# Kernel tuning notes

Measured on AMD Instinct MI355X. Metric: run time of the kernel, lower is better.

The kernel has to match this reference:

```python
import jax, jax.numpy as jnp
import numpy as np

NUM_USERS = 100000
NUM_ITEMS = 50000
N_TOTAL = NUM_USERS + NUM_ITEMS
NNZ = 4000000
LATENT_DIM = 64
N_LAYERS = 3
BATCH = 16384


def setup_inputs() -> dict:
    key = jax.random.key(0)
    k1, k2, k3, k4, k5, k6, k7 = jax.random.split(key, 7)
    return {
        "user_emb": jax.random.normal(k1, (NUM_USERS, LATENT_DIM), dtype=jnp.float32) * 0.1,
        "item_emb": jax.random.normal(k2, (NUM_ITEMS, LATENT_DIM), dtype=jnp.float32) * 0.1,
        "vals": jax.random.uniform(k3, (NNZ,), dtype=jnp.float32),
        "rows": jax.random.randint(k4, (NNZ,), 0, N_TOTAL, dtype=jnp.int32),
        "cols": jax.random.randint(k5, (NNZ,), 0, N_TOTAL, dtype=jnp.int32),
        "users": jax.random.randint(k6, (BATCH,), 0, NUM_USERS, dtype=jnp.int64),
        "items": jax.random.randint(k7, (BATCH,), 0, NUM_ITEMS, dtype=jnp.int64),
    }


def _spmm(vals, rows, cols, x):
    # sparse.mm(A, x) with A given as COO edge list: out[r] += vals * x[c]
    return jax.ops.segment_sum(vals[:, None] * x[cols], rows, num_segments=N_TOTAL)


def reference(user_emb, item_emb, vals, rows, cols, users, items):
    # LightGCN.computer(): multi-hop propagation + mean over layer outputs
    all_emb = jnp.concatenate([user_emb, item_emb], axis=0)  # [N+M, d]
    acc = all_emb
    emb = all_emb
    for _ in range(N_LAYERS):
        emb = _spmm(vals, rows, cols, emb)
        acc = acc + emb
    light_out = acc / jnp.asarray(N_LAYERS + 1, dtype=acc.dtype)
    all_users = light_out[:NUM_USERS]
    all_items = light_out[NUM_USERS:]
    # forward(users, items): gather and elementwise dot product
    u = all_users[users]  # [B, d]
    i = all_items[items]  # [B, d]
    gamma = jnp.sum(u * i, axis=1)  # [B]
    return gamma
```

## Files before the change

### kernel.cpp

```cpp
#include <hip/hip_runtime.h>

#define NUM_USERS 100000
#define NUM_ITEMS 50000
#define N_TOTAL   150000
#define LATENT    64
#define BATCH     16384
#define BROWS     512
#define NB        293
#define CAP       16384
#define P1_T      512
#define P1_C      4096

typedef unsigned int u32;
typedef unsigned short u16;

__device__ __forceinline__ u16 f32_to_bf16(float f) {
    u32 u = __float_as_uint(f);
    u32 r = (u + 0x7FFFu + ((u >> 16) & 1u)) >> 16;
    return (u16)r;
}
__device__ __forceinline__ float bf16_lo(u32 w) { return __uint_as_float(w << 16); }
__device__ __forceinline__ float bf16_hi(u32 w) { return __uint_as_float(w & 0xFFFF0000u); }

__device__ __forceinline__ void fma4(float acc[4], uint2 xv, float v) {
    acc[0] = fmaf(v, bf16_lo(xv.x), acc[0]);
    acc[1] = fmaf(v, bf16_hi(xv.x), acc[1]);
    acc[2] = fmaf(v, bf16_lo(xv.y), acc[2]);
    acc[3] = fmaf(v, bf16_hi(xv.y), acc[3]);
}

__device__ __forceinline__ int wave_incl_scan(int v, int lane) {
    #pragma unroll
    for (int d = 1; d < 64; d <<= 1) {
        int t = __shfl_up(v, d, 64);
        if (lane >= d) v += t;
    }
    return v;
}

__device__ __forceinline__ int block_excl_scan_512(int v, int t, int* wsum) {
    int lane = t & 63, w = t >> 6;
    int incl = wave_incl_scan(v, lane);
    if (lane == 63) wsum[w] = incl;
    __syncthreads();
    if (t == 0) {
        int acc = 0;
        #pragma unroll
        for (int k = 0; k < 8; ++k) { int c = wsum[k]; wsum[k] = acc; acc += c; }
    }
    __syncthreads();
    return wsum[w] + incl - v;
}

__global__ void __launch_bounds__(P1_T)
partition1_kernel(const int* __restrict__ rows, const int* __restrict__ cols,
                  const float* __restrict__ vals,
                  int* __restrict__ ccur, uint2* __restrict__ packed0,
                  u16* __restrict__ klab, int nnz) {
    __shared__ u32 skey[P1_C];
    __shared__ u32 sval[P1_C];
    __shared__ u16 sbucket[P1_C];
    __shared__ int cnt[NB];
    __shared__ int lstart[NB];
    __shared__ int lcur[NB];
    __shared__ int gbase[NB];
    __shared__ int wsum[8];

    int t = threadIdx.x;
    int base = blockIdx.x * P1_C;
    int chunkN = nnz - base; if (chunkN > P1_C) chunkN = P1_C;

    for (int i = t; i < NB; i += P1_T) cnt[i] = 0;
    __syncthreads();

    int er[8]; u32 ek[8]; u32 ev[8];
    #pragma unroll
    for (int k = 0; k < 8; ++k) {
        int e = base + k * P1_T + t;
        bool ok = (k * P1_T + t) < chunkN;
        int r = ok ? rows[e] : 0;
        er[k] = ok ? (r >> 9) : -1;
        if (ok) {
            ek[k] = (u32)cols[e] | ((u32)(r & (BROWS - 1)) << 18);
            ev[k] = __float_as_uint(vals[e]);
            atomicAdd(&cnt[er[k]], 1);
        }
    }
    __syncthreads();

    int v = (t < NB) ? cnt[t] : 0;
    int excl = block_excl_scan_512(v, t, wsum);
    if (t < NB) {
        lstart[t] = excl;
        lcur[t] = excl;
        gbase[t] = v ? atomicAdd(&ccur[t], v) : 0;
    }
    __syncthreads();

    #pragma unroll
    for (int k = 0; k < 8; ++k) {
        if (er[k] >= 0) {
            int pos = atomicAdd(&lcur[er[k]], 1);
            skey[pos] = ek[k];
            sval[pos] = ev[k];
            sbucket[pos] = (u16)er[k];
        }
    }
    __syncthreads();

    for (int idx = t; idx < chunkN; idx += P1_T) {
        int b2 = sbucket[idx];
        size_t gp = (size_t)b2 * CAP + gbase[b2] + (idx - lstart[b2]);
        u32 key = skey[idx];
        packed0[gp] = make_uint2(key, sval[idx]);
        klab[gp] = (u16)(key >> 18);
    }
}

__global__ void bucket_scan_kernel(const int* __restrict__ ccur, int* __restrict__ cptr,
                                   int* __restrict__ rowptr, int nnz) {
    __shared__ int wsum[8];
    int t = threadIdx.x;
    int v = (t < NB) ? ccur[t] : 0;
    int excl = block_excl_scan_512(v, t, wsum);
    if (t < NB) cptr[t] = excl;
    if (t == 0) { cptr[NB] = nnz; rowptr[N_TOTAL] = nnz; }
}

__global__ void __launch_bounds__(BROWS)
partition2_kernel(const int* __restrict__ cptr, const uint2* __restrict__ packed0,
                  const u16* __restrict__ klab,
                  uint2* __restrict__ edges, int* __restrict__ rowptr) {
    __shared__ int cnt[BROWS];
    __shared__ int cur[BROWS];
    __shared__ int wsum[8];
    int b = blockIdx.x;
    int t = threadIdx.x;
    const uint2* src = packed0 + (size_t)b * CAP;
    const u16*   kl  = klab + (size_t)b * CAP;
    int outb = cptr[b];
    int count = cptr[b + 1] - outb;
    cnt[t] = 0;
    __syncthreads();
    for (int i = t; i < count; i += 2 * BROWS) {
        u16 k0 = kl[i];
        int i2 = i + BROWS;
        if (i2 < count) {
            u16 k1 = kl[i2];
            atomicAdd(&cnt[k0], 1);
            atomicAdd(&cnt[k1], 1);
        } else {
            atomicAdd(&cnt[k0], 1);
        }
    }
    __syncthreads();
    int v = cnt[t];
    int excl = block_excl_scan_512(v, t, wsum);
    cur[t] = excl;
    int r = (b << 9) + t;
    if (r < N_TOTAL) rowptr[r] = outb + excl;
    __syncthreads();
    for (int i = t; i < count; i += 2 * BROWS) {
        uint2 p0 = src[i];
        int i2 = i + BROWS;
        if (i2 < count) {
            uint2 p1 = src[i2];
            int pos0 = outb + atomicAdd(&cur[p0.x >> 18], 1);
            int pos1 = outb + atomicAdd(&cur[p1.x >> 18], 1);
            edges[pos0] = make_uint2(p0.x & 0x3FFFFu, p0.y);
            edges[pos1] = make_uint2(p1.x & 0x3FFFFu, p1.y);
        } else {
            int pos0 = outb + atomicAdd(&cur[p0.x >> 18], 1);
            edges[pos0] = make_uint2(p0.x & 0x3FFFFu, p0.y);
        }
    }
}

__global__ void convert_kernel(const float* __restrict__ ue, const float* __restrict__ ie,
                               u16* __restrict__ x) {
    int i = blockIdx.x * blockDim.x + threadIdx.x;
    const int n4 = N_TOTAL * LATENT / 4;
    const int ub = NUM_USERS * LATENT / 4;
    if (i >= n4) return;
    float4 f = (i < ub) ? reinterpret_cast<const float4*>(ue)[i]
                        : reinterpret_cast<const float4*>(ie)[i - ub];
    ushort4 o;
    o.x = f32_to_bf16(f.x); o.y = f32_to_bf16(f.y);
    o.z = f32_to_bf16(f.z); o.w = f32_to_bf16(f.w);
    reinterpret_cast<ushort4*>(x)[i] = o;
}

__device__ __forceinline__ void row_tail(const uint2* __restrict__ edges,
                                         const u16* __restrict__ x,
                                         int i, int e, int j, int q, float acc[4]) {
    for (; i + 8 <= e; i += 8) {
        uint2 e0 = edges[i + j];
        uint2 e1 = edges[i + 4 + j];
        uint2 x0 = *reinterpret_cast<const uint2*>(x + (size_t)e0.x * LATENT + q);
        uint2 x1 = *reinterpret_cast<const uint2*>(x + (size_t)e1.x * LATENT + q);
        fma4(acc, x0, __uint_as_float(e0.y));
        fma4(acc, x1, __uint_as_float(e1.y));
    }
    for (; i < e; i += 4) {
        uint2 e0 = edges[i + j];
        float v0 = (i + j < e) ? __uint_as_float(e0.y) : 0.f;
        uint2 x0 = *reinterpret_cast<const uint2*>(x + (size_t)e0.x * LATENT + q);
        fma4(acc, x0, v0);
    }
}

__device__ __forceinline__ void spmm_row(const uint2* __restrict__ edges,
                                         const u16* __restrict__ x,
                                         int s, int e, int lane, float acc[4]) {
    int j = lane >> 4;
    int q = (lane & 15) << 2;
    acc[0] = acc[1] = acc[2] = acc[3] = 0.f;
    int i = s;
    for (; i + 16 <= e; i += 16) {
        uint2 e0 = edges[i + j];
        uint2 e1 = edges[i + 4 + j];
        uint2 e2 = edges[i + 8 + j];
        uint2 e3 = edges[i + 12 + j];
        uint2 x0 = *reinterpret_cast<const uint2*>(x + (size_t)e0.x * LATENT + q);
        uint2 x1 = *reinterpret_cast<const uint2*>(x + (size_t)e1.x * LATENT + q);
        uint2 x2 = *reinterpret_cast<const uint2*>(x + (size_t)e2.x * LATENT + q);
        uint2 x3 = *reinterpret_cast<const uint2*>(x + (size_t)e3.x * LATENT + q);
        fma4(acc, x0, __uint_as_float(e0.y));
        fma4(acc, x1, __uint_as_float(e1.y));
        fma4(acc, x2, __uint_as_float(e2.y));
        fma4(acc, x3, __uint_as_float(e3.y));
    }
    row_tail(edges, x, i, e, j, q, acc);
    #pragma unroll
    for (int k = 0; k < 4; ++k) {
        acc[k] += __shfl_xor(acc[k], 16, 64);
        acc[k] += __shfl_xor(acc[k], 32, 64);
    }
}

__global__ void spmm_kernel(const int* __restrict__ rowptr, const uint2* __restrict__ edges,
                            const u16* __restrict__ x, u16* __restrict__ y) {
    int wid = blockIdx.x * 4 + (threadIdx.x >> 6);
    int r0 = wid * 2;
    int lane = threadIdx.x & 63;
    int j = lane >> 4;
    int q = (lane & 15) << 2;
    int i0 = rowptr[r0];
    int e0 = rowptr[r0 + 1];
    int i1 = e0;
    int e1 = rowptr[r0 + 2];
    float a0[4] = {0.f, 0.f, 0.f, 0.f};
    float a1[4] = {0.f, 0.f, 0.f, 0.f};

    while (i0 + 8 <= e0 && i1 + 8 <= e1) {
        uint2 p00 = edges[i0 + j];
        uint2 p01 = edges[i0 + 4 + j];
        uint2 p10 = edges[i1 + j];
        uint2 p11 = edges[i1 + 4 + j];
        uint2 g00 = *reinterpret_cast<const uint2*>(x + (size_t)p00.x * LATENT + q);
        uint2 g01 = *reinterpret_cast<const uint2*>(x + (size_t)p01.x * LATENT + q);
        uint2 g10 = *reinterpret_cast<const uint2*>(x + (size_t)p10.x * LATENT + q);
        uint2 g11 = *reinterpret_cast<const uint2*>(x + (size_t)p11.x * LATENT + q);
        fma4(a0, g00, __uint_as_float(p00.y));
        fma4(a0, g01, __uint_as_float(p01.y));
        fma4(a1, g10, __uint_as_float(p10.y));
        fma4(a1, g11, __uint_as_float(p11.y));
        i0 += 8;
        i1 += 8;
    }
    row_tail(edges, x, i0, e0, j, q, a0);
    row_tail(edges, x, i1, e1, j, q, a1);

    #pragma unroll
    for (int k = 0; k < 4; ++k) {
        a0[k] += __shfl_xor(a0[k], 16, 64);
        a0[k] += __shfl_xor(a0[k], 32, 64);
        a1[k] += __shfl_xor(a1[k], 16, 64);
        a1[k] += __shfl_xor(a1[k], 32, 64);
    }
    if (lane < 16) {
        u32 w0 = (u32)f32_to_bf16(a0[0]) | ((u32)f32_to_bf16(a0[1]) << 16);
        u32 w1 = (u32)f32_to_bf16(a0[2]) | ((u32)f32_to_bf16(a0[3]) << 16);
        *reinterpret_cast<uint2*>(y + (size_t)r0 * LATENT + (lane << 2)) = make_uint2(w0, w1);
        u32 w2 = (u32)f32_to_bf16(a1[0]) | ((u32)f32_to_bf16(a1[1]) << 16);
        u32 w3 = (u32)f32_to_bf16(a1[2]) | ((u32)f32_to_bf16(a1[3]) << 16);
        *reinterpret_cast<uint2*>(y + (size_t)(r0 + 1) * LATENT + (lane << 2)) = make_uint2(w2, w3);
    }
}

__global__ void spmm_batch_kernel(const int* __restrict__ rowptr, const uint2* __restrict__ edges,
                                  const u16* __restrict__ x,
                                  const int* __restrict__ users, const int* __restrict__ items,
                                  float* __restrict__ u_acc, float* __restrict__ i_acc) {
    int slot = blockIdx.x * 4 + (threadIdx.x >> 6);
    int lane = threadIdx.x & 63;
    int row = (slot < BATCH) ? users[slot] : (NUM_USERS + items[slot - BATCH]);
    int s = rowptr[row], e = rowptr[row + 1];
    float acc[4];
    spmm_row(edges, x, s, e, lane, acc);
    if (lane < 16) {
        float* dst = (slot < BATCH) ? (u_acc + (size_t)slot * LATENT)
                                    : (i_acc + (size_t)(slot - BATCH) * LATENT);
        float4* p = reinterpret_cast<float4*>(dst + (lane << 2));
        float4 old = *p;
        *p = make_float4(old.x + acc[0], old.y + acc[1], old.z + acc[2], old.w + acc[3]);
    }
}

__global__ void init_acc_kernel(const float* __restrict__ user_emb,
                                const float* __restrict__ item_emb,
                                const int* __restrict__ users,
                                const int* __restrict__ items,
                                float* __restrict__ u_acc,
                                float* __restrict__ i_acc) {
    int tid = blockIdx.x * blockDim.x + threadIdx.x;
    int b = tid >> 6, d = tid & 63;
    if (b >= BATCH) return;
    u_acc[tid] = user_emb[(size_t)users[b] * LATENT + d];
    i_acc[tid] = item_emb[(size_t)items[b] * LATENT + d];
}

__global__ void gather_acc_kernel(const u16* __restrict__ emb,
                                  const int* __restrict__ users,
                                  const int* __restrict__ items,
                                  float* __restrict__ u_acc,
                                  float* __restrict__ i_acc) {
    int tid = blockIdx.x * blockDim.x + threadIdx.x;
    int b = tid >> 6, d = tid & 63;
    if (b >= BATCH) return;
    u_acc[tid] += __uint_as_float(((u32)emb[(size_t)users[b] * LATENT + d]) << 16);
    i_acc[tid] += __uint_as_float(((u32)emb[((size_t)items[b] + NUM_USERS) * LATENT + d]) << 16);
}

__global__ void dot_kernel(const float* __restrict__ u_acc,
                           const float* __restrict__ i_acc,
                           float* __restrict__ out) {
    int b = blockIdx.x;
    int d = threadIdx.x;
    float p = u_acc[b * 64 + d] * i_acc[b * 64 + d];
    #pragma unroll
    for (int off = 32; off; off >>= 1) p += __shfl_down(p, off, 64);
    if (d == 0) out[b] = p * (1.0f / 16.0f);
}

extern "C" void kernel_launch(void* const* d_in, const int* in_sizes, int n_in,
                              void* d_out, int out_size, void* d_ws, size_t ws_size,
                              hipStream_t stream) {
    const float* user_emb = (const float*)d_in[0];
    const float* item_emb = (const float*)d_in[1];
    const float* vals     = (const float*)d_in[2];
    const int*   rows     = (const int*)d_in[3];
    const int*   cols     = (const int*)d_in[4];
    const int*   users    = (const int*)d_in[5];
    const int*   items    = (const int*)d_in[6];
    float* out = (float*)d_out;

    const int nnz = in_sizes[2];

    char* ws = (char*)d_ws;
    const size_t embB   = (size_t)N_TOTAL * LATENT * sizeof(u16);
    const size_t accB   = (size_t)BATCH * LATENT * sizeof(float);
    const size_t slabB  = (size_t)NB * CAP * sizeof(uint2);
    const size_t klabB  = (size_t)NB * CAP * sizeof(u16);
    const size_t edgeB  = (size_t)(nnz + 16) * sizeof(uint2);

    size_t off = 0;
    u16*   emb_a   = (u16*)  (ws + off); off += embB;
    u16*   emb_b   = (u16*)  (ws + off); off += embB;
    uint2* packed0 = (uint2*)(ws + off); off += slabB;
    u16*   klab    = (u16*)  (ws + off); off += klabB;
    uint2* edges   = (uint2*)(ws + off); off += edgeB;
    float* u_acc   = (float*)(ws + off); off += accB;
    float* i_acc   = (float*)(ws + off); off += accB;
    int*   rowptr  = (int*)  (ws + off); off += (size_t)(N_TOTAL + 1) * sizeof(int);
    int*   ccur    = (int*)  (ws + off); off += (size_t)(NB + 1) * sizeof(int);
    int*   cptr    = (int*)  (ws + off); off += (size_t)(NB + 1) * sizeof(int);

    hipMemsetAsync(ccur, 0, (size_t)(NB + 1) * sizeof(int), stream);
    hipMemsetAsync(edges + nnz, 0, 16 * sizeof(uint2), stream);
    partition1_kernel<<<(nnz + P1_C - 1) / P1_C, P1_T, 0, stream>>>(
        rows, cols, vals, ccur, packed0, klab, nnz);
    bucket_scan_kernel<<<1, 512, 0, stream>>>(ccur, cptr, rowptr, nnz);
    partition2_kernel<<<NB, BROWS, 0, stream>>>(cptr, packed0, klab, edges, rowptr);

    convert_kernel<<<(N_TOTAL * LATENT / 4 + 255) / 256, 256, 0, stream>>>(
        user_emb, item_emb, emb_a);
    init_acc_kernel<<<(BATCH * 64) / 256, 256, 0, stream>>>(
        user_emb, item_emb, users, items, u_acc, i_acc);

    u16* cur = emb_a;
    u16* nxt = emb_b;
    for (int l = 0; l < 2; ++l) {
        spmm_kernel<<<N_TOTAL / 8, 256, 0, stream>>>(rowptr, edges, cur, nxt);
        gather_acc_kernel<<<(BATCH * 64) / 256, 256, 0, stream>>>(
            nxt, users, items, u_acc, i_acc);
        u16* t = cur; cur = nxt; nxt = t;
    }

    spmm_batch_kernel<<<(2 * BATCH) / 4, 256, 0, stream>>>(
        rowptr, edges, cur, users, items, u_acc, i_acc);

    dot_kernel<<<BATCH, 64, 0, stream>>>(u_acc, i_acc, out);
}
```

Measured before the change: 304.7 us.

## Fuse independent setup kernels and gather steps into fewer launches

Merges partition1, embedding conversion and accumulator init into one kernel whose blocks take different roles by block index. The bucket scan moves into every partition2 block, which removes a single-block launch. The layer gathers are folded into the following spmm launch or into spmm_batch, and dot_kernel packs 8 batch rows per block. This cuts roughly seven launches and their serialization gaps, at the cost of redundant scans and heterogeneous blocks sharing one launch configuration and shared-memory footprint.

```diff
diff --git a/kernel.cpp b/kernel.cpp
--- a/kernel.cpp
+++ b/kernel.cpp
@@ -10,6 +10,9 @@
 #define CAP       16384
 #define P1_T      512
 #define P1_C      4096
+#define CVT_B     2344
+#define INIT_B    512
+#define GATH_B    1024
 
 typedef unsigned int u32;
 typedef unsigned short u16;
@@ -53,10 +56,14 @@
 }
 
 __global__ void __launch_bounds__(P1_T)
-partition1_kernel(const int* __restrict__ rows, const int* __restrict__ cols,
-                  const float* __restrict__ vals,
-                  int* __restrict__ ccur, uint2* __restrict__ packed0,
-                  u16* __restrict__ klab, int nnz) {
+fatA_kernel(const int* __restrict__ rows, const int* __restrict__ cols,
+            const float* __restrict__ vals,
+            int* __restrict__ ccur, uint2* __restrict__ packed0, u16* __restrict__ klab,
+            const float* __restrict__ ue, const float* __restrict__ ie,
+            u16* __restrict__ emb0,
+            const int* __restrict__ users, const int* __restrict__ items,
+            float* __restrict__ u_acc, float* __restrict__ i_acc,
+            int nnz, int np1) {
     __shared__ u32 skey[P1_C];
     __shared__ u32 sval[P1_C];
     __shared__ u16 sbucket[P1_C];
@@ -67,81 +74,107 @@
     __shared__ int wsum[8];
 
     int t = threadIdx.x;
-    int base = blockIdx.x * P1_C;
-    int chunkN = nnz - base; if (chunkN > P1_C) chunkN = P1_C;
-
-    for (int i = t; i < NB; i += P1_T) cnt[i] = 0;
-    __syncthreads();
-
-    int er[8]; u32 ek[8]; u32 ev[8];
-    #pragma unroll
-    for (int k = 0; k < 8; ++k) {
-        int e = base + k * P1_T + t;
-        bool ok = (k * P1_T + t) < chunkN;
-        int r = ok ? rows[e] : 0;
-        er[k] = ok ? (r >> 9) : -1;
-        if (ok) {
-            ek[k] = (u32)cols[e] | ((u32)(r & (BROWS - 1)) << 18);
-            ev[k] = __float_as_uint(vals[e]);
-            atomicAdd(&cnt[er[k]], 1);
-        }
-    }
-    __syncthreads();
-
-    int v = (t < NB) ? cnt[t] : 0;
-    int excl = block_excl_scan_512(v, t, wsum);
-    if (t < NB) {
-        lstart[t] = excl;
-        lcur[t] = excl;
-        gbase[t] = v ? atomicAdd(&ccur[t], v) : 0;
-    }
-    __syncthreads();
-
-    #pragma unroll
-    for (int k = 0; k < 8; ++k) {
-        if (er[k] >= 0) {
-            int pos = atomicAdd(&lcur[er[k]], 1);
-            skey[pos] = ek[k];
-            sval[pos] = ev[k];
-            sbucket[pos] = (u16)er[k];
-        }
-    }
-    __syncthreads();
-
-    for (int idx = t; idx < chunkN; idx += P1_T) {
-        int b2 = sbucket[idx];
-        size_t gp = (size_t)b2 * CAP + gbase[b2] + (idx - lstart[b2]);
-        u32 key = skey[idx];
-        packed0[gp] = make_uint2(key, sval[idx]);
-        klab[gp] = (u16)(key >> 18);
-    }
-}
-
-__global__ void bucket_scan_kernel(const int* __restrict__ ccur, int* __restrict__ cptr,
-                                   int* __restrict__ rowptr, int nnz) {
-    __shared__ int wsum[8];
-    int t = threadIdx.x;
-    int v = (t < NB) ? ccur[t] : 0;
-    int excl = block_excl_scan_512(v, t, wsum);
-    if (t < NB) cptr[t] = excl;
-    if (t == 0) { cptr[NB] = nnz; rowptr[N_TOTAL] = nnz; }
+    int bid = blockIdx.x;
+
+    if (bid < np1) {
+        int base = bid * P1_C;
+        int chunkN = nnz - base; if (chunkN > P1_C) chunkN = P1_C;
+
+        for (int i = t; i < NB; i += P1_T) cnt[i] = 0;
+        __syncthreads();
+
+        int er[8]; u32 ek[8]; u32 ev[8];
+        #pragma unroll
+        for (int k = 0; k < 8; ++k) {
+            int e = base + k * P1_T + t;
+            bool ok = (k * P1_T + t) < chunkN;
+            int r = ok ? rows[e] : 0;
+            er[k] = ok ? (r >> 9) : -1;
+            if (ok) {
+                ek[k] = (u32)cols[e] | ((u32)(r & (BROWS - 1)) << 18);
+                ev[k] = __float_as_uint(vals[e]);
+                atomicAdd(&cnt[er[k]], 1);
+            }
+        }
+        __syncthreads();
+
+        int v = (t < NB) ? cnt[t] : 0;
+        int excl = block_excl_scan_512(v, t, wsum);
+        if (t < NB) {
+            lstart[t] = excl;
+            lcur[t] = excl;
+            gbase[t] = v ? atomicAdd(&ccur[t], v) : 0;
+        }
+        __syncthreads();
+
+        #pragma unroll
+        for (int k = 0; k < 8; ++k) {
+            if (er[k] >= 0) {
+                int pos = atomicAdd(&lcur[er[k]], 1);
+                skey[pos] = ek[k];
+                sval[pos] = ev[k];
+                sbucket[pos] = (u16)er[k];
+            }
+        }
+        __syncthreads();
+
+        for (int idx = t; idx < chunkN; idx += P1_T) {
+            int b2 = sbucket[idx];
+            size_t gp = (size_t)b2 * CAP + gbase[b2] + (idx - lstart[b2]);
+            u32 key = skey[idx];
+            packed0[gp] = make_uint2(key, sval[idx]);
+            klab[gp] = (u16)(key >> 18);
+        }
+    } else if (bid < np1 + CVT_B) {
+        const int n4 = N_TOTAL * LATENT / 4;
+        const int ub = NUM_USERS * LATENT / 4;
+        const int T  = CVT_B * P1_T;
+        int g = (bid - np1) * P1_T + t;
+        #pragma unroll
+        for (int rep = 0; rep < 2; ++rep) {
+            int i = g + rep * T;
+            if (i < n4) {
+                float4 f = (i < ub) ? reinterpret_cast<const float4*>(ue)[i]
+                                    : reinterpret_cast<const float4*>(ie)[i - ub];
+                ushort4 o;
+                o.x = f32_to_bf16(f.x); o.y = f32_to_bf16(f.y);
+                o.z = f32_to_bf16(f.z); o.w = f32_to_bf16(f.w);
+                reinterpret_cast<ushort4*>(emb0)[i] = o;
+            }
+        }
+    } else {
+        int g = (bid - np1 - CVT_B) * P1_T + t;
+        int b = g >> 4, dq = (g & 15) << 2;
+        if (b < BATCH) {
+            reinterpret_cast<float4*>(u_acc + (size_t)b * LATENT + dq)[0] =
+                reinterpret_cast<const float4*>(ue + (size_t)users[b] * LATENT + dq)[0];
+            reinterpret_cast<float4*>(i_acc + (size_t)b * LATENT + dq)[0] =
+                reinterpret_cast<const float4*>(ie + (size_t)items[b] * LATENT + dq)[0];
+        }
+    }
 }
 
 __global__ void __launch_bounds__(BROWS)
-partition2_kernel(const int* __restrict__ cptr, const uint2* __restrict__ packed0,
+partition2_kernel(const int* __restrict__ ccur, const uint2* __restrict__ packed0,
                   const u16* __restrict__ klab,
-                  uint2* __restrict__ edges, int* __restrict__ rowptr) {
+                  uint2* __restrict__ edges, int* __restrict__ rowptr, int nnz) {
     __shared__ int cnt[BROWS];
     __shared__ int cur[BROWS];
     __shared__ int wsum[8];
+    __shared__ int sOutb;
     int b = blockIdx.x;
     int t = threadIdx.x;
+
+    int cv = (t < NB) ? ccur[t] : 0;
+    int cexcl = block_excl_scan_512(cv, t, wsum);
+    if (t == b) sOutb = cexcl;
+    cnt[t] = 0;
+    __syncthreads();
+    int outb = sOutb;
+    int count = ccur[b];
+
     const uint2* src = packed0 + (size_t)b * CAP;
     const u16*   kl  = klab + (size_t)b * CAP;
-    int outb = cptr[b];
-    int count = cptr[b + 1] - outb;
-    cnt[t] = 0;
-    __syncthreads();
     for (int i = t; i < count; i += 2 * BROWS) {
         u16 k0 = kl[i];
         int i2 = i + BROWS;
@@ -159,6 +192,7 @@
     cur[t] = excl;
     int r = (b << 9) + t;
     if (r < N_TOTAL) rowptr[r] = outb + excl;
+    if (b == NB - 1 && t == 0) rowptr[N_TOTAL] = nnz;
     __syncthreads();
     for (int i = t; i < count; i += 2 * BROWS) {
         uint2 p0 = src[i];
@@ -174,20 +208,6 @@
             edges[pos0] = make_uint2(p0.x & 0x3FFFFu, p0.y);
         }
     }
-}
-
-__global__ void convert_kernel(const float* __restrict__ ue, const float* __restrict__ ie,
-                               u16* __restrict__ x) {
-    int i = blockIdx.x * blockDim.x + threadIdx.x;
-    const int n4 = N_TOTAL * LATENT / 4;
-    const int ub = NUM_USERS * LATENT / 4;
-    if (i >= n4) return;
-    float4 f = (i < ub) ? reinterpret_cast<const float4*>(ue)[i]
-                        : reinterpret_cast<const float4*>(ie)[i - ub];
-    ushort4 o;
-    o.x = f32_to_bf16(f.x); o.y = f32_to_bf16(f.y);
-    o.z = f32_to_bf16(f.z); o.w = f32_to_bf16(f.w);
-    reinterpret_cast<ushort4*>(x)[i] = o;
 }
 
 __device__ __forceinline__ void row_tail(const uint2* __restrict__ edges,
@@ -238,11 +258,12 @@
     }
 }
 
-__global__ void spmm_kernel(const int* __restrict__ rowptr, const uint2* __restrict__ edges,
-                            const u16* __restrict__ x, u16* __restrict__ y) {
-    int wid = blockIdx.x * 4 + (threadIdx.x >> 6);
+__device__ __forceinline__ void spmm_two_rows(const int* __restrict__ rowptr,
+                                              const uint2* __restrict__ edges,
+                                              const u16* __restrict__ x,
+                                              u16* __restrict__ y,
+                                              int wid, int lane) {
     int r0 = wid * 2;
-    int lane = threadIdx.x & 63;
     int j = lane >> 4;
     int q = (lane & 15) << 2;
     int i0 = rowptr[r0];
@@ -288,6 +309,43 @@
     }
 }
 
+__device__ __forceinline__ void gather_role(const u16* __restrict__ emb,
+                                            const int* __restrict__ users,
+                                            const int* __restrict__ items,
+                                            float* __restrict__ u_acc,
+                                            float* __restrict__ i_acc, int g) {
+    int b = g >> 4, dq = (g & 15) << 2;
+    if (b >= BATCH) return;
+    uint2 xu = *reinterpret_cast<const uint2*>(emb + (size_t)users[b] * LATENT + dq);
+    uint2 xi = *reinterpret_cast<const uint2*>(emb + ((size_t)items[b] + NUM_USERS) * LATENT + dq);
+    float4* pu = reinterpret_cast<float4*>(u_acc + (size_t)b * LATENT + dq);
+    float4* pi = reinterpret_cast<float4*>(i_acc + (size_t)b * LATENT + dq);
+    float4 ou = *pu, oi = *pi;
+    ou.x += bf16_lo(xu.x); ou.y += bf16_hi(xu.x); ou.z += bf16_lo(xu.y); ou.w += bf16_hi(xu.y);
+    oi.x += bf16_lo(xi.x); oi.y += bf16_hi(xi.x); oi.z += bf16_lo(xi.y); oi.w += bf16_hi(xi.y);
+    *pu = ou; *pi = oi;
+}
+
+__global__ void spmm_kernel(const int* __restrict__ rowptr, const uint2* __restrict__ edges,
+                            const u16* __restrict__ x, u16* __restrict__ y) {
+    int wid = blockIdx.x * 4 + (threadIdx.x >> 6);
+    spmm_two_rows(rowptr, edges, x, y, wid, threadIdx.x & 63);
+}
+
+__global__ void spmm_gather_kernel(const int* __restrict__ rowptr, const uint2* __restrict__ edges,
+                                   const u16* __restrict__ x, u16* __restrict__ y,
+                                   const int* __restrict__ users, const int* __restrict__ items,
+                                   float* __restrict__ u_acc, float* __restrict__ i_acc,
+                                   int nspmm) {
+    int bid = blockIdx.x;
+    if (bid < nspmm) {
+        int wid = bid * 4 + (threadIdx.x >> 6);
+        spmm_two_rows(rowptr, edges, x, y, wid, threadIdx.x & 63);
+    } else {
+        gather_role(x, users, items, u_acc, i_acc, (bid - nspmm) * 256 + threadIdx.x);
+    }
+}
+
 __global__ void spmm_batch_kernel(const int* __restrict__ rowptr, const uint2* __restrict__ edges,
                                   const u16* __restrict__ x,
                                   const int* __restrict__ users, const int* __restrict__ items,
@@ -299,44 +357,24 @@
     float acc[4];
     spmm_row(edges, x, s, e, lane, acc);
     if (lane < 16) {
+        uint2 xr = *reinterpret_cast<const uint2*>(x + (size_t)row * LATENT + (lane << 2));
         float* dst = (slot < BATCH) ? (u_acc + (size_t)slot * LATENT)
                                     : (i_acc + (size_t)(slot - BATCH) * LATENT);
         float4* p = reinterpret_cast<float4*>(dst + (lane << 2));
         float4 old = *p;
-        *p = make_float4(old.x + acc[0], old.y + acc[1], old.z + acc[2], old.w + acc[3]);
-    }
-}
-
-__global__ void init_acc_kernel(const float* __restrict__ user_emb,
-                                const float* __restrict__ item_emb,
-                                const int* __restrict__ users,
-                                const int* __restrict__ items,
-                                float* __restrict__ u_acc,
-                                float* __restrict__ i_acc) {
-    int tid = blockIdx.x * blockDim.x + threadIdx.x;
-    int b = tid >> 6, d = tid & 63;
-    if (b >= BATCH) return;
-    u_acc[tid] = user_emb[(size_t)users[b] * LATENT + d];
-    i_acc[tid] = item_emb[(size_t)items[b] * LATENT + d];
-}
-
-__global__ void gather_acc_kernel(const u16* __restrict__ emb,
-                                  const int* __restrict__ users,
-                                  const int* __restrict__ items,
-                                  float* __restrict__ u_acc,
-                                  float* __restrict__ i_acc) {
-    int tid = blockIdx.x * blockDim.x + threadIdx.x;
-    int b = tid >> 6, d = tid & 63;
-    if (b >= BATCH) return;
-    u_acc[tid] += __uint_as_float(((u32)emb[(size_t)users[b] * LATENT + d]) << 16);
-    i_acc[tid] += __uint_as_float(((u32)emb[((size_t)items[b] + NUM_USERS) * LATENT + d]) << 16);
+        old.x += acc[0] + bf16_lo(xr.x);
+        old.y += acc[1] + bf16_hi(xr.x);
+        old.z += acc[2] + bf16_lo(xr.y);
+        old.w += acc[3] + bf16_hi(xr.y);
+        *p = old;
+    }
 }
 
 __global__ void dot_kernel(const float* __restrict__ u_acc,
                            const float* __restrict__ i_acc,
                            float* __restrict__ out) {
-    int b = blockIdx.x;
-    int d = threadIdx.x;
+    int b = blockIdx.x * 8 + (threadIdx.x >> 6);
+    int d = threadIdx.x & 63;
     float p = u_acc[b * 64 + d] * i_acc[b * 64 + d];
     #pragma unroll
     for (int off = 32; off; off >>= 1) p += __shfl_down(p, off, 64);
@@ -356,6 +394,7 @@
     float* out = (float*)d_out;
 
     const int nnz = in_sizes[2];
+    const int np1 = (nnz + P1_C - 1) / P1_C;
 
     char* ws = (char*)d_ws;
     const size_t embB   = (size_t)N_TOTAL * LATENT * sizeof(u16);
@@ -374,31 +413,21 @@
     float* i_acc   = (float*)(ws + off); off += accB;
     int*   rowptr  = (int*)  (ws + off); off += (size_t)(N_TOTAL + 1) * sizeof(int);
     int*   ccur    = (int*)  (ws + off); off += (size_t)(NB + 1) * sizeof(int);
-    int*   cptr    = (int*)  (ws + off); off += (size_t)(NB + 1) * sizeof(int);
 
     hipMemsetAsync(ccur, 0, (size_t)(NB + 1) * sizeof(int), stream);
     hipMemsetAsync(edges + nnz, 0, 16 * sizeof(uint2), stream);
-    partition1_kernel<<<(nnz + P1_C - 1) / P1_C, P1_T, 0, stream>>>(
-        rows, cols, vals, ccur, packed0, klab, nnz);
-    bucket_scan_kernel<<<1, 512, 0, stream>>>(ccur, cptr, rowptr, nnz);
-    partition2_kernel<<<NB, BROWS, 0, stream>>>(cptr, packed0, klab, edges, rowptr);
-
-    convert_kernel<<<(N_TOTAL * LATENT / 4 + 255) / 256, 256, 0, stream>>>(
-        user_emb, item_emb, emb_a);
-    init_acc_kernel<<<(BATCH * 64) / 256, 256, 0, stream>>>(
-        user_emb, item_emb, users, items, u_acc, i_acc);
-
-    u16* cur = emb_a;
-    u16* nxt = emb_b;
-    for (int l = 0; l < 2; ++l) {
-        spmm_kernel<<<N_TOTAL / 8, 256, 0, stream>>>(rowptr, edges, cur, nxt);
-        gather_acc_kernel<<<(BATCH * 64) / 256, 256, 0, stream>>>(
-            nxt, users, items, u_acc, i_acc);
-        u16* t = cur; cur = nxt; nxt = t;
-    }
-
+
+    fatA_kernel<<<np1 + CVT_B + INIT_B, P1_T, 0, stream>>>(
+        rows, cols, vals, ccur, packed0, klab,
+        user_emb, item_emb, emb_a, users, items, u_acc, i_acc, nnz, np1);
+
+    partition2_kernel<<<NB, BROWS, 0, stream>>>(ccur, packed0, klab, edges, rowptr, nnz);
+
+    spmm_kernel<<<N_TOTAL / 8, 256, 0, stream>>>(rowptr, edges, emb_a, emb_b);
+    spmm_gather_kernel<<<N_TOTAL / 8 + GATH_B, 256, 0, stream>>>(
+        rowptr, edges, emb_b, emb_a, users, items, u_acc, i_acc, N_TOTAL / 8);
     spmm_batch_kernel<<<(2 * BATCH) / 4, 256, 0, stream>>>(
-        rowptr, edges, cur, users, items, u_acc, i_acc);
-
-    dot_kernel<<<BATCH, 64, 0, stream>>>(u_acc, i_acc, out);
-}
+        rowptr, edges, emb_a, users, items, u_acc, i_acc);
+
+    dot_kernel<<<BATCH / 8, 512, 0, stream>>>(u_acc, i_acc, out);
+}
```

Result: faster. 287.3 us (-5.7%).
